# Optimization experiments

Hardware: AMD Instinct MI355X
Metric: run time of the kernel (lower is better)

The kernel has to match this reference:

```python
import jax, jax.numpy as jnp
from jax import lax
import numpy as np

B, S, I, H = 64, 1024, 1024, 1024


def setup_inputs() -> dict:
    key = jax.random.key(0)
    k1, k2, k3, k4 = jax.random.split(key, 4)
    scale = 1.0 / np.sqrt(H)
    return {
        "x": jax.random.normal(k1, (B, S, I), dtype=jnp.float32),
        "h0": jnp.zeros((B, H), dtype=jnp.float32),
        "W_ih": jax.random.normal(k2, (3 * H, I), dtype=jnp.float32) * scale,
        "W_hh": jax.random.normal(k3, (3 * H, H), dtype=jnp.float32) * scale,
        "b_ih": jax.random.normal(k4, (3 * H,), dtype=jnp.float32) * scale,
    }


def reference(x, h0, W_ih, W_hh, b_ih):
    # Standard GRUCell math with bias_ih=True, bias_hh=False.
    # Precompute all input-to-hidden projections in one big GEMM: [B,S,3H]
    gi_all = jnp.einsum("bsi,gi->bsg", x, W_ih) + b_ih

    def step(h, gi):
        gh = h @ W_hh.T                      # [B, 3H]
        i_r, i_z, i_n = jnp.split(gi, 3, axis=-1)
        h_r, h_z, h_n = jnp.split(gh, 3, axis=-1)
        r = jax.nn.sigmoid(i_r + h_r)
        z = jax.nn.sigmoid(i_z + h_z)
        n = jnp.tanh(i_n + r * h_n)
        h_new = (1.0 - z) * n + z * h
        return h_new, h_new

    hx, ys = lax.scan(step, h0, jnp.swapaxes(gi_all, 0, 1))  # ys: [S,B,H]
    output = jnp.swapaxes(ys, 0, 1)  # [B,S,H]
    return output, hx
```

## Files before the change

### kernel.cpp

```cpp
#include <hip/hip_runtime.h>
#include <hip/hip_bf16.h>
#include <cstdint>
#include <cstddef>

#define BB 64
#define SS 1024
#define II 1024
#define HH 1024
#define G3 3072

typedef float  f32x4  __attribute__((ext_vector_type(4)));
typedef short  bf16x8 __attribute__((ext_vector_type(8)));

__device__ __forceinline__ unsigned short f2b(float f) {
    unsigned u = __float_as_uint(f);
    u += 0x7FFFu + ((u >> 16) & 1u);
    return (unsigned short)(u >> 16);
}
__device__ __forceinline__ float b2f(unsigned short s) {
    return __uint_as_float(((unsigned)s) << 16);
}

__global__ __launch_bounds__(256)
void conv_b16(const float* __restrict__ x, const float* __restrict__ w,
              unsigned short* __restrict__ xb, unsigned short* __restrict__ wb)
{
    const size_t XN = (size_t)BB * SS * II;
    const size_t WN = (size_t)G3 * II;
    size_t i = ((size_t)blockIdx.x * 256 + threadIdx.x) * 4;
    if (i < XN) {
        float4 v = *reinterpret_cast<const float4*>(x + i);
        uint2 p;
        p.x = (unsigned)f2b(v.x) | ((unsigned)f2b(v.y) << 16);
        p.y = (unsigned)f2b(v.z) | ((unsigned)f2b(v.w) << 16);
        *reinterpret_cast<uint2*>(xb + i) = p;
    } else {
        size_t j = i - XN;
        if (j < WN) {
            float4 v = *reinterpret_cast<const float4*>(w + j);
            uint2 p;
            p.x = (unsigned)f2b(v.x) | ((unsigned)f2b(v.y) << 16);
            p.y = (unsigned)f2b(v.z) | ((unsigned)f2b(v.w) << 16);
            *reinterpret_cast<uint2*>(wb + j) = p;
        }
    }
}

__global__ __launch_bounds__(256)
void gru_init(const float* __restrict__ h0, unsigned short* __restrict__ h16,
              int* __restrict__ flags)
{
    int i = blockIdx.x * 256 + threadIdx.x;
    int b = i >> 10, j = i & 1023;
    int dst = (b >> 4) * 16384 + (j >> 3) * 128 + (b & 15) * 8 + (j & 7);
    h16[dst] = f2b(h0[i]);
    if (i < 2304) flags[i] = 0;
}

__global__ __launch_bounds__(512, 1)
void gru_fused(float* __restrict__ gi, const unsigned short* __restrict__ XB,
               const unsigned short* __restrict__ WB, const float* __restrict__ bias,
               const float* __restrict__ Whh, const float* __restrict__ h0,
               unsigned short* __restrict__ h16, int* __restrict__ flags,
               float* __restrict__ out)
{
    __shared__ char smem[52224];
    const int t    = threadIdx.x;
    const int lane = t & 63;
    const int wave = t >> 6;
    const int bid  = blockIdx.x;

    if (bid >= 128) {
        short* As = (short*)smem;
        short* Bs = (short*)(smem + 16384);
        const int wkr = bid - 128;
        const int lr  = lane >> 3;
        const int lc  = (lane & 7) * 8;
        const int mb  = (wave & 1) * 64;
        const int nb  = (wave >> 1) * 32;

        for (int kjob = 0; kjob < 96; ++kjob) {
            int j  = wkr + (kjob << 7);
            int sc = j / 1536, r = j - sc * 1536;
            int b  = r / 24,   n = r - b * 24;
            int m0 = b * 1024 + sc * 128;
            int n0 = n * 128;

            f32x4 acc[4][2] = {};
            for (int k0 = 0; k0 < II; k0 += 64) {
                __syncthreads();
                #pragma unroll
                for (int p = 0; p < 2; ++p) {
                    int sg = p * 8 + wave;
                    const unsigned short* ga = XB + (size_t)(m0 + sg * 8 + lr) * II + k0 + lc;
                    const unsigned short* gb = WB + (size_t)(n0 + sg * 8 + lr) * II + k0 + lc;
                    __builtin_amdgcn_global_load_lds(
                        (const __attribute__((address_space(1))) void*)ga,
                        (__attribute__((address_space(3))) void*)(As + sg * 512), 16, 0, 0);
                    __builtin_amdgcn_global_load_lds(
                        (const __attribute__((address_space(1))) void*)gb,
                        (__attribute__((address_space(3))) void*)(Bs + sg * 512), 16, 0, 0);
                }
                __syncthreads();
                #pragma unroll
                for (int ks = 0; ks < 2; ++ks) {
                    bf16x8 af[4], bf[2];
                    #pragma unroll
                    for (int i = 0; i < 4; ++i)
                        af[i] = *reinterpret_cast<const bf16x8*>(
                            As + (mb + i * 16 + (lane & 15)) * 64 + ks * 32 + (lane >> 4) * 8);
                    #pragma unroll
                    for (int i = 0; i < 2; ++i)
                        bf[i] = *reinterpret_cast<const bf16x8*>(
                            Bs + (nb + i * 16 + (lane & 15)) * 64 + ks * 32 + (lane >> 4) * 8);
                    #pragma unroll
                    for (int mi = 0; mi < 4; ++mi)
                        #pragma unroll
                        for (int ni = 0; ni < 2; ++ni)
                            acc[mi][ni] = __builtin_amdgcn_mfma_f32_16x16x32_bf16(
                                af[mi], bf[ni], acc[mi][ni], 0, 0, 0);
                }
            }
            #pragma unroll
            for (int ni = 0; ni < 2; ++ni) {
                int ncol = n0 + nb + ni * 16 + (lane & 15);
                float bv = bias[ncol];
                #pragma unroll
                for (int mi = 0; mi < 4; ++mi) {
                    int mrow = m0 + mb + mi * 16 + ((lane >> 4) << 2);
                    #pragma unroll
                    for (int e = 0; e < 4; ++e) {
                        float v = acc[mi][ni][e] + bv;
                        __hip_atomic_store(
                            (unsigned*)(gi + (size_t)(mrow + e) * G3 + ncol),
                            __float_as_uint(v), __ATOMIC_RELAXED,
                            __HIP_MEMORY_SCOPE_AGENT);
                    }
                }
            }
            if ((kjob % 12) == 11) {
                asm volatile("s_waitcnt vmcnt(0)" ::: "memory");
                __syncthreads();
                if (t == 0)
                    __hip_atomic_fetch_add(&flags[2048 + (sc << 4)], 1,
                                           __ATOMIC_RELAXED, __HIP_MEMORY_SCOPE_AGENT);
            }
        }
        return;
    }

    auto part = reinterpret_cast<float(*)[6][4][68]>(smem);

    const int group = bid & 3;
    const int jb    = bid >> 2;

    bf16x8 wf[4][6];
    #pragma unroll
    for (int kc = 0; kc < 4; ++kc) {
        #pragma unroll
        for (int nt = 0; nt < 6; ++nt) {
            int rowg = (nt >> 1) * HH + jb * 32 + (nt & 1) * 16 + (lane & 15);
            int k    = wave * 128 + kc * 32 + ((lane >> 4) << 3);
            const float4* src = reinterpret_cast<const float4*>(Whh + (size_t)rowg * HH + k);
            float4 f0 = src[0], f1 = src[1];
            bf16x8 w;
            w[0] = (short)f2b(f0.x); w[1] = (short)f2b(f0.y);
            w[2] = (short)f2b(f0.z); w[3] = (short)f2b(f0.w);
            w[4] = (short)f2b(f1.x); w[5] = (short)f2b(f1.y);
            w[6] = (short)f2b(f1.z); w[7] = (short)f2b(f1.w);
            wf[kc][nt] = w;
        }
    }

    const int b_l = t >> 5;
    const int j_l = t & 31;
    const int b_g = (group << 4) + b_l;
    const int j_g = (jb << 5) + j_l;
    float hreg = h0[b_g * HH + j_g];

    const int frag_base = (wave * 16 + (lane >> 4)) * 256 + ((lane & 15) << 4);
    const int prod_off  = ((j_g >> 3) << 8) + (b_l << 4) + ((j_g & 7) << 1);

    const int nt_r = j_l >> 4;
    const int lp   = ((b_l >> 2) << 4) | (j_l & 15);
    const int e_r  = b_l & 3;

    const int poll_fi = ((group << 5) | (wave << 2) | (lane & 3)) << 4;

    for (int s = 0; s < SS; ++s) {
        if ((s & 127) == 0) {
            if (t == 0) {
                while (__hip_atomic_load(&flags[2048 + ((s >> 7) << 4)],
                                         __ATOMIC_RELAXED, __HIP_MEMORY_SCOPE_AGENT) < 128)
                    __builtin_amdgcn_s_sleep(2);
            }
            __syncthreads();
        }

        const int p = s & 1;
        const char* rslab = (const char*)(h16 + (size_t)p * 65536 + group * 16384);
        unsigned short* wslab = h16 + (size_t)(p ^ 1) * 65536 + group * 16384;

        size_t gib = ((size_t)b_g * SS + s) * G3;
        float ir  = __uint_as_float(__hip_atomic_load(
            (const unsigned*)(gi + gib + j_g), __ATOMIC_RELAXED, __HIP_MEMORY_SCOPE_AGENT));
        float iz  = __uint_as_float(__hip_atomic_load(
            (const unsigned*)(gi + gib + HH + j_g), __ATOMIC_RELAXED, __HIP_MEMORY_SCOPE_AGENT));
        float inn = __uint_as_float(__hip_atomic_load(
            (const unsigned*)(gi + gib + 2 * HH + j_g), __ATOMIC_RELAXED, __HIP_MEMORY_SCOPE_AGENT));

        if (s > 0) {
            while (true) {
                int v = __hip_atomic_load(&flags[poll_fi], __ATOMIC_RELAXED,
                                          __HIP_MEMORY_SCOPE_AGENT);
                if (__all(v >= s)) break;
            }
            asm volatile("" ::: "memory");
        }

        unsigned long long hv[8];
        #pragma unroll
        for (int kc = 0; kc < 4; ++kc) {
            const unsigned long long* q =
                (const unsigned long long*)(rslab + frag_base + kc * 1024);
            hv[2 * kc]     = __hip_atomic_load(q,     __ATOMIC_RELAXED,
                                               __HIP_MEMORY_SCOPE_AGENT);
            hv[2 * kc + 1] = __hip_atomic_load(q + 1, __ATOMIC_RELAXED,
                                               __HIP_MEMORY_SCOPE_AGENT);
        }

        f32x4 acc[6] = {};
        #pragma unroll
        for (int kc = 0; kc < 4; ++kc) {
            union { unsigned long long q[2]; bf16x8 v; } u;
            u.q[0] = hv[2 * kc]; u.q[1] = hv[2 * kc + 1];
            #pragma unroll
            for (int nt = 0; nt < 6; ++nt)
                acc[nt] = __builtin_amdgcn_mfma_f32_16x16x32_bf16(u.v, wf[kc][nt], acc[nt], 0, 0, 0);
        }

        #pragma unroll
        for (int nt = 0; nt < 6; ++nt)
            #pragma unroll
            for (int e = 0; e < 4; ++e)
                part[wave][nt][e][lane] = acc[nt][e];
        __syncthreads();

        float hr = 0.f, hz = 0.f, hn = 0.f;
        #pragma unroll
        for (int w = 0; w < 8; ++w) {
            hr += part[w][0 + nt_r][e_r][lp];
            hz += part[w][2 + nt_r][e_r][lp];
            hn += part[w][4 + nt_r][e_r][lp];
        }

        float r  = __builtin_amdgcn_rcpf(1.f + __expf(-(ir + hr)));
        float z  = __builtin_amdgcn_rcpf(1.f + __expf(-(iz + hz)));
        float e2 = __expf(2.f * (inn + r * hn));
        float n  = 1.f - 2.f * __builtin_amdgcn_rcpf(e2 + 1.f);
        float hnew = (1.f - z) * n + z * hreg;
        hreg = hnew;

        unsigned short myb = f2b(hnew);
        unsigned pv = (unsigned)__shfl_xor((int)(unsigned)myb, 1);
        if (!(j_l & 1)) {
            unsigned val = ((unsigned)myb) | (pv << 16);
            __hip_atomic_store((unsigned*)((char*)wslab + prod_off), val,
                               __ATOMIC_RELAXED, __HIP_MEMORY_SCOPE_AGENT);
        }

        asm volatile("s_waitcnt vmcnt(0)" ::: "memory");
        __syncthreads();
        if (t == 0)
            __hip_atomic_store(&flags[((group << 5) | jb) << 4], s + 1,
                               __ATOMIC_RELAXED, __HIP_MEMORY_SCOPE_AGENT);

        out[((size_t)b_g * SS + s) * HH + j_g] = hnew;
    }

    out[(size_t)BB * SS * HH + (size_t)b_g * HH + j_g] = hreg;
}

template<int GI_BF16>
__global__ __launch_bounds__(256)
void gi_gemm(const float* __restrict__ X, const float* __restrict__ W,
             const float* __restrict__ bias, void* __restrict__ gi_out)
{
    __shared__ short As[128][40];
    __shared__ short Bs[128][40];

    const int t    = threadIdx.x;
    const int lane = t & 63;
    const int wave = t >> 6;
    const int m0   = blockIdx.y * 128;
    const int n0   = blockIdx.x * 128;

    f32x4 acc[4][4] = {};

    for (int k0 = 0; k0 < II; k0 += 32) {
        __syncthreads();
        #pragma unroll
        for (int q = 0; q < 2; ++q) {
            int row = (t >> 2) + 64 * q;
            int col = (t & 3) * 8;
            const float4* ap = reinterpret_cast<const float4*>(X + (size_t)(m0 + row) * II + k0 + col);
            const float4* bp = reinterpret_cast<const float4*>(W + (size_t)(n0 + row) * II + k0 + col);
            float4 a0 = ap[0], a1 = ap[1];
            float4 b0 = bp[0], b1 = bp[1];
            bf16x8 av, bv;
            av[0] = (short)f2b(a0.x); av[1] = (short)f2b(a0.y);
            av[2] = (short)f2b(a0.z); av[3] = (short)f2b(a0.w);
            av[4] = (short)f2b(a1.x); av[5] = (short)f2b(a1.y);
            av[6] = (short)f2b(a1.z); av[7] = (short)f2b(a1.w);
            bv[0] = (short)f2b(b0.x); bv[1] = (short)f2b(b0.y);
            bv[2] = (short)f2b(b0.z); bv[3] = (short)f2b(b0.w);
            bv[4] = (short)f2b(b1.x); bv[5] = (short)f2b(b1.y);
            bv[6] = (short)f2b(b1.z); bv[7] = (short)f2b(b1.w);
            *reinterpret_cast<bf16x8*>(&As[row][col]) = av;
            *reinterpret_cast<bf16x8*>(&Bs[row][col]) = bv;
        }
        __syncthreads();

        const int mb = (wave & 1) * 64;
        const int nb = (wave >> 1) * 64;
        bf16x8 af[4], bf[4];
        #pragma unroll
        for (int i = 0; i < 4; ++i) {
            af[i] = *reinterpret_cast<const bf16x8*>(&As[mb + i * 16 + (lane & 15)][(lane >> 4) * 8]);
            bf[i] = *reinterpret_cast<const bf16x8*>(&Bs[nb + i * 16 + (lane & 15)][(lane >> 4) * 8]);
        }
        #pragma unroll
        for (int mi = 0; mi < 4; ++mi)
            #pragma unroll
            for (int ni = 0; ni < 4; ++ni)
                acc[mi][ni] = __builtin_amdgcn_mfma_f32_16x16x32_bf16(af[mi], bf[ni], acc[mi][ni], 0, 0, 0);
    }

    const int mb = (wave & 1) * 64;
    const int nb = (wave >> 1) * 64;
    #pragma unroll
    for (int ni = 0; ni < 4; ++ni) {
        int ncol = n0 + nb + ni * 16 + (lane & 15);
        float bv = bias[ncol];
        #pragma unroll
        for (int mi = 0; mi < 4; ++mi) {
            int mrow = m0 + mb + mi * 16 + ((lane >> 4) << 2);
            #pragma unroll
            for (int e = 0; e < 4; ++e) {
                float v = acc[mi][ni][e] + bv;
                size_t idx = (size_t)(mrow + e) * G3 + ncol;
                if (GI_BF16) ((unsigned short*)gi_out)[idx] = f2b(v);
                else         ((float*)gi_out)[idx] = v;
            }
        }
    }
}

template<int GI_BF16>
__global__ __launch_bounds__(512, 1)
void gru_scan(const void* __restrict__ gi_v, const float* __restrict__ Whh,
              const float* __restrict__ h0, unsigned short* __restrict__ h16,
              int* __restrict__ flags, float* __restrict__ out)
{
    const int t     = threadIdx.x;
    const int lane  = t & 63;
    const int wave  = t >> 6;
    const int bid   = blockIdx.x;
    const int group = bid & 3;
    const int jb    = bid >> 2;

    __shared__ float part[8][6][4][68];

    bf16x8 wf[4][6];
    #pragma unroll
    for (int kc = 0; kc < 4; ++kc) {
        #pragma unroll
        for (int nt = 0; nt < 6; ++nt) {
            int rowg = (nt >> 1) * HH + jb * 32 + (nt & 1) * 16 + (lane & 15);
            int k    = wave * 128 + kc * 32 + ((lane >> 4) << 3);
            const float4* src = reinterpret_cast<const float4*>(Whh + (size_t)rowg * HH + k);
            float4 f0 = src[0], f1 = src[1];
            bf16x8 w;
            w[0] = (short)f2b(f0.x); w[1] = (short)f2b(f0.y);
            w[2] = (short)f2b(f0.z); w[3] = (short)f2b(f0.w);
            w[4] = (short)f2b(f1.x); w[5] = (short)f2b(f1.y);
            w[6] = (short)f2b(f1.z); w[7] = (short)f2b(f1.w);
            wf[kc][nt] = w;
        }
    }

    const int b_l = t >> 5;
    const int j_l = t & 31;
    const int b_g = (group << 4) + b_l;
    const int j_g = (jb << 5) + j_l;
    float hreg = h0[b_g * HH + j_g];

    const int frag_base = (wave * 16 + (lane >> 4)) * 256 + ((lane & 15) << 4);
    const int prod_off  = ((j_g >> 3) << 8) + (b_l << 4) + ((j_g & 7) << 1);

    const int nt_r = j_l >> 4;
    const int lp   = ((b_l >> 2) << 4) | (j_l & 15);
    const int e_r  = b_l & 3;

    const int poll_fi = ((group << 5) | (wave << 2) | (lane & 3)) << 4;

    for (int s = 0; s < SS; ++s) {
        const int p = s & 1;
        const char* rslab = (const char*)(h16 + (size_t)p * 65536 + group * 16384);
        unsigned short* wslab = h16 + (size_t)(p ^ 1) * 65536 + group * 16384;

        size_t gib = ((size_t)b_g * SS + s) * G3;
        float ir, iz, inn;
        if (GI_BF16) {
            const unsigned short* g16 = (const unsigned short*)gi_v;
            ir  = b2f(g16[gib + j_g]);
            iz  = b2f(g16[gib + HH + j_g]);
            inn = b2f(g16[gib + 2 * HH + j_g]);
        } else {
            const float* g32 = (const float*)gi_v;
            ir  = g32[gib + j_g];
            iz  = g32[gib + HH + j_g];
            inn = g32[gib + 2 * HH + j_g];
        }

        if (s > 0) {
            while (true) {
                int v = __hip_atomic_load(&flags[poll_fi], __ATOMIC_RELAXED,
                                          __HIP_MEMORY_SCOPE_AGENT);
                if (__all(v >= s)) break;
            }
            asm volatile("" ::: "memory");
        }

        unsigned long long hv[8];
        #pragma unroll
        for (int kc = 0; kc < 4; ++kc) {
            const unsigned long long* q =
                (const unsigned long long*)(rslab + frag_base + kc * 1024);
            hv[2 * kc]     = __hip_atomic_load(q,     __ATOMIC_RELAXED,
                                               __HIP_MEMORY_SCOPE_AGENT);
            hv[2 * kc + 1] = __hip_atomic_load(q + 1, __ATOMIC_RELAXED,
                                               __HIP_MEMORY_SCOPE_AGENT);
        }

        f32x4 acc[6] = {};
        #pragma unroll
        for (int kc = 0; kc < 4; ++kc) {
            union { unsigned long long q[2]; bf16x8 v; } u;
            u.q[0] = hv[2 * kc]; u.q[1] = hv[2 * kc + 1];
            #pragma unroll
            for (int nt = 0; nt < 6; ++nt)
                acc[nt] = __builtin_amdgcn_mfma_f32_16x16x32_bf16(u.v, wf[kc][nt], acc[nt], 0, 0, 0);
        }

        #pragma unroll
        for (int nt = 0; nt < 6; ++nt)
            #pragma unroll
            for (int e = 0; e < 4; ++e)
                part[wave][nt][e][lane] = acc[nt][e];
        __syncthreads();

        float hr = 0.f, hz = 0.f, hn = 0.f;
        #pragma unroll
        for (int w = 0; w < 8; ++w) {
            hr += part[w][0 + nt_r][e_r][lp];
            hz += part[w][2 + nt_r][e_r][lp];
            hn += part[w][4 + nt_r][e_r][lp];
        }

        float r  = __builtin_amdgcn_rcpf(1.f + __expf(-(ir + hr)));
        float z  = __builtin_amdgcn_rcpf(1.f + __expf(-(iz + hz)));
        float e2 = __expf(2.f * (inn + r * hn));
        float n  = 1.f - 2.f * __builtin_amdgcn_rcpf(e2 + 1.f);
        float hnew = (1.f - z) * n + z * hreg;
        hreg = hnew;

        unsigned short myb = f2b(hnew);
        unsigned pv = (unsigned)__shfl_xor((int)(unsigned)myb, 1);
        if (!(j_l & 1)) {
            unsigned val = ((unsigned)myb) | (pv << 16);
            __hip_atomic_store((unsigned*)((char*)wslab + prod_off), val,
                               __ATOMIC_RELAXED, __HIP_MEMORY_SCOPE_AGENT);
        }

        asm volatile("s_waitcnt vmcnt(0)" ::: "memory");
        __syncthreads();
        if (t == 0)
            __hip_atomic_store(&flags[((group << 5) | jb) << 4], s + 1,
                               __ATOMIC_RELAXED, __HIP_MEMORY_SCOPE_AGENT);

        out[((size_t)b_g * SS + s) * HH + j_g] = hnew;
    }

    out[(size_t)BB * SS * HH + (size_t)b_g * HH + j_g] = hreg;
}

extern "C" void kernel_launch(void* const* d_in, const int* in_sizes, int n_in,
                              void* d_out, int out_size, void* d_ws, size_t ws_size,
                              hipStream_t stream)
{
    const float* x   = (const float*)d_in[0];
    const float* h0  = (const float*)d_in[1];
    const float* Wih = (const float*)d_in[2];
    const float* Whh = (const float*)d_in[3];
    const float* bih = (const float*)d_in[4];
    float* out = (float*)d_out;

    char* ws = (char*)d_ws;
    unsigned short* h16 = (unsigned short*)ws;
    int* flags          = (int*)(ws + 262144);
    void* gi            = (void*)(ws + (1 << 20));

    const size_t gi32_bytes = (size_t)BB * SS * G3 * 4;
    const size_t gi16_bytes = gi32_bytes / 2;
    const size_t xb_off   = (size_t)(1 << 20) + gi32_bytes;
    const size_t wb_off   = xb_off + (size_t)BB * SS * II * 2;
    const size_t need_new = wb_off + (size_t)G3 * II * 2;

    const bool use_new = ws_size >= need_new;
    const bool use_f32 = !use_new && ws_size >= ((size_t)(1 << 20) + gi32_bytes);
    const bool use_b16 = !use_new && !use_f32 &&
                         ws_size >= ((size_t)(1 << 20) + gi16_bytes);
    if (!use_new && !use_f32 && !use_b16) return;

    gru_init<<<dim3(256), dim3(256), 0, stream>>>(h0, h16, flags);

    if (use_new) {
        unsigned short* xb = (unsigned short*)(ws + xb_off);
        unsigned short* wb = (unsigned short*)(ws + wb_off);
        conv_b16<<<dim3(68608), dim3(256), 0, stream>>>(x, Wih, xb, wb);
        float* gi_f = (float*)gi;
        const unsigned short* xb_c = xb;
        const unsigned short* wb_c = wb;
        const float* bih_c = bih;
        const float* Whh_c = Whh;
        const float* h0_c = h0;
        unsigned short* h16_c = h16;
        int* flags_c = flags;
        float* out_c = out;
        void* args[] = { (void*)&gi_f, (void*)&xb_c, (void*)&wb_c, (void*)&bih_c,
                         (void*)&Whh_c, (void*)&h0_c, (void*)&h16_c,
                         (void*)&flags_c, (void*)&out_c };
        hipLaunchCooperativeKernel((const void*)&gru_fused, dim3(256), dim3(512),
                                   args, 0, stream);
    } else {
        const void* gi_c = gi;
        const float* Whh_c = Whh;
        const float* h0_c = h0;
        unsigned short* h16_c = h16;
        int* flags_c = flags;
        float* out_c = out;
        void* args[] = { (void*)&gi_c, (void*)&Whh_c, (void*)&h0_c,
                         (void*)&h16_c, (void*)&flags_c, (void*)&out_c };
        if (use_f32) {
            gi_gemm<0><<<dim3(24, 512), dim3(256), 0, stream>>>(x, Wih, bih, gi);
            hipLaunchCooperativeKernel((const void*)&gru_scan<0>, dim3(128), dim3(512),
                                       args, 0, stream);
        } else {
            gi_gemm<1><<<dim3(24, 512), dim3(256), 0, stream>>>(x, Wih, bih, gi);
            hipLaunchCooperativeKernel((const void*)&gru_scan<1>, dim3(128), dim3(512),
                                       args, 0, stream);
        }
    }
}
```

Baseline: 3.386 ms.

## Compute first GI chunk on all blocks and store GI projections as bf16

```diff
diff --git a/kernel.cpp b/kernel.cpp
--- a/kernel.cpp
+++ b/kernel.cpp
@@ -57,8 +57,77 @@
     if (i < 2304) flags[i] = 0;
 }
 
+__device__ __forceinline__ void gemm_tile(
+    const unsigned short* __restrict__ XB, const unsigned short* __restrict__ WB,
+    const float* __restrict__ bias, unsigned short* __restrict__ gi16,
+    short* As, short* Bs, int m0, int n0, int t, int lane, int wave)
+{
+    const int lr = lane >> 3;
+    const int lc = (lane & 7) * 8;
+    const int mb = (wave & 1) * 64;
+    const int nb = (wave >> 1) * 32;
+
+    f32x4 acc[4][2] = {};
+    for (int k0 = 0; k0 < II; k0 += 64) {
+        __syncthreads();
+        #pragma unroll
+        for (int p = 0; p < 2; ++p) {
+            int sg = p * 8 + wave;
+            const unsigned short* ga = XB + (size_t)(m0 + sg * 8 + lr) * II + k0 + lc;
+            const unsigned short* gb = WB + (size_t)(n0 + sg * 8 + lr) * II + k0 + lc;
+            __builtin_amdgcn_global_load_lds(
+                (const __attribute__((address_space(1))) void*)ga,
+                (__attribute__((address_space(3))) void*)(As + sg * 512), 16, 0, 0);
+            __builtin_amdgcn_global_load_lds(
+                (const __attribute__((address_space(1))) void*)gb,
+                (__attribute__((address_space(3))) void*)(Bs + sg * 512), 16, 0, 0);
+        }
+        __syncthreads();
+        #pragma unroll
+        for (int ks = 0; ks < 2; ++ks) {
+            bf16x8 af[4], bf[2];
+            #pragma unroll
+            for (int i = 0; i < 4; ++i)
+                af[i] = *reinterpret_cast<const bf16x8*>(
+                    As + (mb + i * 16 + (lane & 15)) * 64 + ks * 32 + (lane >> 4) * 8);
+            #pragma unroll
+            for (int i = 0; i < 2; ++i)
+                bf[i] = *reinterpret_cast<const bf16x8*>(
+                    Bs + (nb + i * 16 + (lane & 15)) * 64 + ks * 32 + (lane >> 4) * 8);
+            #pragma unroll
+            for (int mi = 0; mi < 4; ++mi)
+                #pragma unroll
+                for (int ni = 0; ni < 2; ++ni)
+                    acc[mi][ni] = __builtin_amdgcn_mfma_f32_16x16x32_bf16(
+                        af[mi], bf[ni], acc[mi][ni], 0, 0, 0);
+        }
+    }
+    #pragma unroll
+    for (int ni = 0; ni < 2; ++ni) {
+        int ncol = n0 + nb + ni * 16 + (lane & 15);
+        float bv = bias[ncol];
+        #pragma unroll
+        for (int mi = 0; mi < 4; ++mi) {
+            int mrow = m0 + mb + mi * 16 + ((lane >> 4) << 2);
+            #pragma unroll
+            for (int e = 0; e < 4; ++e) {
+                float v = acc[mi][ni][e] + bv;
+                unsigned short hb = f2b(v);
+                unsigned pv = (unsigned)__shfl_xor((int)(unsigned)hb, 1);
+                if (!(lane & 1)) {
+                    unsigned word = (unsigned)hb | (pv << 16);
+                    __hip_atomic_store(
+                        (unsigned*)(gi16 + (size_t)(mrow + e) * G3 + ncol),
+                        word, __ATOMIC_RELAXED, __HIP_MEMORY_SCOPE_AGENT);
+                }
+            }
+        }
+    }
+}
+
 __global__ __launch_bounds__(512, 1)
-void gru_fused(float* __restrict__ gi, const unsigned short* __restrict__ XB,
+void gru_fused(unsigned short* __restrict__ gi16,
+               const unsigned short* __restrict__ XB,
                const unsigned short* __restrict__ WB, const float* __restrict__ bias,
                const float* __restrict__ Whh, const float* __restrict__ h0,
                unsigned short* __restrict__ h16, int* __restrict__ flags,
@@ -70,79 +139,35 @@
     const int wave = t >> 6;
     const int bid  = blockIdx.x;
 
+    short* As = (short*)smem;
+    short* Bs = (short*)(smem + 16384);
+
+    #pragma unroll 1
+    for (int q = 0; q < 6; ++q) {
+        int tile = bid * 6 + q;
+        int b = tile / 24, n = tile % 24;
+        gemm_tile(XB, WB, bias, gi16, As, Bs, b * 1024, n * 128, t, lane, wave);
+    }
+    asm volatile("s_waitcnt vmcnt(0)" ::: "memory");
+    __syncthreads();
+    if (t == 0)
+        __hip_atomic_fetch_add(&flags[2048], 1,
+                               __ATOMIC_RELAXED, __HIP_MEMORY_SCOPE_AGENT);
+
     if (bid >= 128) {
-        short* As = (short*)smem;
-        short* Bs = (short*)(smem + 16384);
         const int wkr = bid - 128;
-        const int lr  = lane >> 3;
-        const int lc  = (lane & 7) * 8;
-        const int mb  = (wave & 1) * 64;
-        const int nb  = (wave >> 1) * 32;
-
-        for (int kjob = 0; kjob < 96; ++kjob) {
-            int j  = wkr + (kjob << 7);
-            int sc = j / 1536, r = j - sc * 1536;
-            int b  = r / 24,   n = r - b * 24;
-            int m0 = b * 1024 + sc * 128;
-            int n0 = n * 128;
-
-            f32x4 acc[4][2] = {};
-            for (int k0 = 0; k0 < II; k0 += 64) {
-                __syncthreads();
-                #pragma unroll
-                for (int p = 0; p < 2; ++p) {
-                    int sg = p * 8 + wave;
-                    const unsigned short* ga = XB + (size_t)(m0 + sg * 8 + lr) * II + k0 + lc;
-                    const unsigned short* gb = WB + (size_t)(n0 + sg * 8 + lr) * II + k0 + lc;
-                    __builtin_amdgcn_global_load_lds(
-                        (const __attribute__((address_space(1))) void*)ga,
-                        (__attribute__((address_space(3))) void*)(As + sg * 512), 16, 0, 0);
-                    __builtin_amdgcn_global_load_lds(
-                        (const __attribute__((address_space(1))) void*)gb,
-                        (__attribute__((address_space(3))) void*)(Bs + sg * 512), 16, 0, 0);
-                }
-                __syncthreads();
-                #pragma unroll
-                for (int ks = 0; ks < 2; ++ks) {
-                    bf16x8 af[4], bf[2];
-                    #pragma unroll
-                    for (int i = 0; i < 4; ++i)
-                        af[i] = *reinterpret_cast<const bf16x8*>(
-                            As + (mb + i * 16 + (lane & 15)) * 64 + ks * 32 + (lane >> 4) * 8);
-                    #pragma unroll
-                    for (int i = 0; i < 2; ++i)
-                        bf[i] = *reinterpret_cast<const bf16x8*>(
-                            Bs + (nb + i * 16 + (lane & 15)) * 64 + ks * 32 + (lane >> 4) * 8);
-                    #pragma unroll
-                    for (int mi = 0; mi < 4; ++mi)
-                        #pragma unroll
-                        for (int ni = 0; ni < 2; ++ni)
-                            acc[mi][ni] = __builtin_amdgcn_mfma_f32_16x16x32_bf16(
-                                af[mi], bf[ni], acc[mi][ni], 0, 0, 0);
-                }
-            }
-            #pragma unroll
-            for (int ni = 0; ni < 2; ++ni) {
-                int ncol = n0 + nb + ni * 16 + (lane & 15);
-                float bv = bias[ncol];
-                #pragma unroll
-                for (int mi = 0; mi < 4; ++mi) {
-                    int mrow = m0 + mb + mi * 16 + ((lane >> 4) << 2);
-                    #pragma unroll
-                    for (int e = 0; e < 4; ++e) {
-                        float v = acc[mi][ni][e] + bv;
-                        __hip_atomic_store(
-                            (unsigned*)(gi + (size_t)(mrow + e) * G3 + ncol),
-                            __float_as_uint(v), __ATOMIC_RELAXED,
-                            __HIP_MEMORY_SCOPE_AGENT);
-                    }
-                }
-            }
-            if ((kjob % 12) == 11) {
+        #pragma unroll 1
+        for (int jj = 0; jj < 84; ++jj) {
+            int c   = 1 + jj / 12;
+            int idx = (jj % 12) * 128 + wkr;
+            int b = idx / 24, n = idx % 24;
+            gemm_tile(XB, WB, bias, gi16, As, Bs,
+                      b * 1024 + c * 128, n * 128, t, lane, wave);
+            if ((jj % 12) == 11) {
                 asm volatile("s_waitcnt vmcnt(0)" ::: "memory");
                 __syncthreads();
                 if (t == 0)
-                    __hip_atomic_fetch_add(&flags[2048 + (sc << 4)], 1,
+                    __hip_atomic_fetch_add(&flags[2048 + (c << 4)], 1,
                                            __ATOMIC_RELAXED, __HIP_MEMORY_SCOPE_AGENT);
             }
         }
@@ -186,12 +211,15 @@
     const int e_r  = b_l & 3;
 
     const int poll_fi = ((group << 5) | (wave << 2) | (lane & 3)) << 4;
+    const int jeven = j_g & ~1;
+    const int jsel  = (j_g & 1) << 4;
 
     for (int s = 0; s < SS; ++s) {
         if ((s & 127) == 0) {
+            const int target = (s == 0) ? 256 : 128;
             if (t == 0) {
                 while (__hip_atomic_load(&flags[2048 + ((s >> 7) << 4)],
-                                         __ATOMIC_RELAXED, __HIP_MEMORY_SCOPE_AGENT) < 128)
+                                         __ATOMIC_RELAXED, __HIP_MEMORY_SCOPE_AGENT) < target)
                     __builtin_amdgcn_s_sleep(2);
             }
             __syncthreads();
@@ -202,12 +230,15 @@
         unsigned short* wslab = h16 + (size_t)(p ^ 1) * 65536 + group * 16384;
 
         size_t gib = ((size_t)b_g * SS + s) * G3;
-        float ir  = __uint_as_float(__hip_atomic_load(
-            (const unsigned*)(gi + gib + j_g), __ATOMIC_RELAXED, __HIP_MEMORY_SCOPE_AGENT));
-        float iz  = __uint_as_float(__hip_atomic_load(
-            (const unsigned*)(gi + gib + HH + j_g), __ATOMIC_RELAXED, __HIP_MEMORY_SCOPE_AGENT));
-        float inn = __uint_as_float(__hip_atomic_load(
-            (const unsigned*)(gi + gib + 2 * HH + j_g), __ATOMIC_RELAXED, __HIP_MEMORY_SCOPE_AGENT));
+        unsigned wr = __hip_atomic_load((const unsigned*)(gi16 + gib + jeven),
+                                        __ATOMIC_RELAXED, __HIP_MEMORY_SCOPE_AGENT);
+        unsigned wz = __hip_atomic_load((const unsigned*)(gi16 + gib + HH + jeven),
+                                        __ATOMIC_RELAXED, __HIP_MEMORY_SCOPE_AGENT);
+        unsigned wn = __hip_atomic_load((const unsigned*)(gi16 + gib + 2 * HH + jeven),
+                                        __ATOMIC_RELAXED, __HIP_MEMORY_SCOPE_AGENT);
+        float ir  = b2f((unsigned short)(wr >> jsel));
+        float iz  = b2f((unsigned short)(wz >> jsel));
+        float inn = b2f((unsigned short)(wn >> jsel));
 
         if (s > 0) {
             while (true) {
@@ -529,7 +560,7 @@
         unsigned short* xb = (unsigned short*)(ws + xb_off);
         unsigned short* wb = (unsigned short*)(ws + wb_off);
         conv_b16<<<dim3(68608), dim3(256), 0, stream>>>(x, Wih, xb, wb);
-        float* gi_f = (float*)gi;
+        unsigned short* gi16_p = (unsigned short*)gi;
         const unsigned short* xb_c = xb;
         const unsigned short* wb_c = wb;
         const float* bih_c = bih;
@@ -538,7 +569,7 @@
         unsigned short* h16_c = h16;
         int* flags_c = flags;
         float* out_c = out;
-        void* args[] = { (void*)&gi_f, (void*)&xb_c, (void*)&wb_c, (void*)&bih_c,
+        void* args[] = { (void*)&gi16_p, (void*)&xb_c, (void*)&wb_c, (void*)&bih_c,
                          (void*)&Whh_c, (void*)&h0_c, (void*)&h16_c,
                          (void*)&flags_c, (void*)&out_c };
         hipLaunchCooperativeKernel((const void*)&gru_fused, dim3(256), dim3(512),
```

Result: faster. 2.985 ms (median of 2 runs) (-11.9%).
